# Kernel tuning notes

Measured on AMD Instinct MI355X. Metric: run time of the kernel, lower is better.

The kernel has to match this reference:

```python
import jax, jax.numpy as jnp
import numpy as np

N, E, G, H, F_IN = 100_000, 3_200_000, 256, 16, 7
RRELU_SLOPE = (1.0 / 8.0 + 1.0 / 3.0) / 2.0  # eval-mode RReLU uses mean slope


def rrelu(x):
    return jnp.where(x >= 0, x, RRELU_SLOPE * x)


def gcn_conv(x, edge_index, edge_weight, W, b, n_nodes):
    """PyG GCNConv: add self-loops, symmetric norm, gather-matmul-scatter."""
    row, col = edge_index[0], edge_index[1]
    loop = jnp.arange(n_nodes)
    row = jnp.concatenate([row, loop])
    col = jnp.concatenate([col, loop])
    w = jnp.concatenate([edge_weight, jnp.ones((n_nodes,), x.dtype)])
    deg = jax.ops.segment_sum(w, col, num_segments=n_nodes)
    dis = jnp.where(deg > 0, jax.lax.rsqrt(jnp.maximum(deg, 1e-12)), 0.0)
    norm = dis[row] * w * dis[col]            # [E+N]
    h = x @ W                                  # [N, out]
    msg = h[row] * norm[:, None]               # gather + scale
    return jax.ops.segment_sum(msg, col, num_segments=n_nodes) + b


def max_pool_neighbor_x(x, edge_index, n_nodes):
    row, col = edge_index[0], edge_index[1]
    loop = jnp.arange(n_nodes)
    row = jnp.concatenate([row, loop])
    col = jnp.concatenate([col, loop])
    return jax.ops.segment_max(x[row], col, num_segments=n_nodes)


def setup_inputs() -> dict:
    key = jax.random.key(0)
    ks = jax.random.split(key, 12)
    x = jax.random.normal(ks[0], (N, F_IN), jnp.float32)
    edge_index = jax.random.randint(ks[1], (2, E), 0, N)
    edge_weights = jax.random.uniform(ks[2], (E,), jnp.float32)
    batch = (jnp.arange(N) * G) // N  # sorted, every graph non-empty
    s = 0.2
    W1 = jax.random.normal(ks[3], (F_IN, H), jnp.float32) * s
    b1 = jnp.zeros((H,), jnp.float32)
    W2 = jax.random.normal(ks[4], (H, H), jnp.float32) * s
    b2 = jnp.zeros((H,), jnp.float32)
    Wl1 = jax.random.normal(ks[5], (H, H), jnp.float32) * s
    bl1 = jax.random.normal(ks[6], (H,), jnp.float32) * s
    Wl3 = jax.random.normal(ks[7], (H, H), jnp.float32) * s
    bl3 = jax.random.normal(ks[8], (H,), jnp.float32) * s
    Wl4 = jax.random.normal(ks[9], (H, 1), jnp.float32) * s
    bl4 = jax.random.normal(ks[10], (1,), jnp.float32) * s
    return {"x": x, "edge_index": edge_index, "batch": batch,
            "edge_weights": edge_weights, "W1": W1, "b1": b1, "W2": W2,
            "b2": b2, "Wl1": Wl1, "bl1": bl1, "Wl3": Wl3, "bl3": bl3,
            "Wl4": Wl4, "bl4": bl4}


def reference(x, edge_index, batch, edge_weights, W1, b1, W2, b2,
              Wl1, bl1, Wl3, bl3, Wl4, bl4):
    h = gcn_conv(x, edge_index, edge_weights, W1, b1, N)
    h = max_pool_neighbor_x(h, edge_index, N)
    res = h
    h = gcn_conv(h, edge_index, jnp.ones((E,), h.dtype), W2, b2, N)
    h = jax.nn.relu(res + h)
    g = jax.ops.segment_max(h, batch, num_segments=G)  # global_max_pool
    res = g
    g = rrelu(res + (g @ Wl1 + bl1))
    res = g
    g = rrelu(res + (g @ Wl3 + bl3))
    # dropout p=0.5 in eval mode -> identity
    g = rrelu(g @ Wl4 + bl4)
    return g
```

## Files before the change

### kernel.cpp

```cpp
#include <hip/hip_runtime.h>
#include <hip/hip_fp16.h>
#include <math.h>

#define NN 100000
#define NE 3200000
#define NG 256
#define HD 16
#define FIN 7

#define RB 8
#define RSZ 256
#define NBUK 391
#define NBUKP 400
#define FB 512
#define CHUNK 6250
#define CH2 3125
#define SCB 8
#define ASTRIDE 17
#define CSTRIDE 9
#define LMASK 0x1FFFF

#define S16 65536.0f
#define INV_S16 1.52587890625e-5f
#define IBIAS 33554432u
#define S_DEGW 16777216.0f
#define INV_S_DEGW 5.9604644775390625e-8f

static constexpr float SLOPE = 0.22916666666666666f;

__device__ __forceinline__ float rrelu_f(float a) {
    return a >= 0.f ? a : SLOPE * a;
}

__device__ __forceinline__ unsigned encf(float v) {
    unsigned u = __float_as_uint(v);
    return u ^ (((unsigned)((int)u >> 31)) | 0x80000000u);
}
__device__ __forceinline__ float decf(unsigned u) {
    unsigned m = ((int)u < 0) ? 0x80000000u : 0xFFFFFFFFu;
    return __uint_as_float(u ^ m);
}
#define ENC_NEGINF 0x00800000u

__device__ __forceinline__ float h2f(unsigned short us) {
    __half h = *(__half*)&us;
    return __half2float(h);
}


__global__ __launch_bounds__(512) void k_hist(
        const int* __restrict__ col, int* __restrict__ hist) {
    __shared__ int bins[NBUK];
    for (int i = threadIdx.x; i < NBUK; i += 512) bins[i] = 0;
    __syncthreads();
    const int2* c2 = (const int2*)(col + blockIdx.x * CHUNK);
    for (int i = threadIdx.x; i < CH2; i += 512) {
        int2 v = c2[i];
        atomicAdd(&bins[v.x >> RB], 1);
        atomicAdd(&bins[v.y >> RB], 1);
    }
    __syncthreads();
    for (int i = threadIdx.x; i < NBUK; i += 512)
        hist[blockIdx.x * NBUKP + i] = bins[i];
}

__global__ __launch_bounds__(512) void k_scan_a(
        const int* __restrict__ hist, int* __restrict__ pre_t,
        int* __restrict__ tot) {
    __shared__ int s[SCB * (FB + 1)];
    int t = threadIdx.x;
    int c0 = blockIdx.x * SCB;
    for (int i = t; i < SCB * FB; i += 512) {
        int j = i >> 3, c = i & 7;
        int cc = c0 + c;
        s[c * (FB + 1) + j] = (cc < NBUK) ? hist[j * NBUKP + cc] : 0;
    }
    __syncthreads();
    int w = t >> 6, l = t & 63;
    int* sb = &s[w * (FB + 1)];
    int base = l * 8;
    int loc[8];
    int run = 0;
#pragma unroll
    for (int k = 0; k < 8; ++k) { loc[k] = run; run += sb[base + k]; }
    int inc = run;
#pragma unroll
    for (int d = 1; d < 64; d <<= 1) {
        int v = __shfl_up(inc, d, 64);
        if (l >= d) inc += v;
    }
    int excl = inc - run;
    int cc = c0 + w;
    if (cc < NBUK) {
#pragma unroll
        for (int k = 0; k < 8; ++k) sb[base + k] = excl + loc[k];
        if (l == 63) tot[cc] = inc;
    }
    __syncthreads();
    for (int i = t; i < SCB * FB; i += 512) {
        int j = i >> 3, c = i & 7;
        int cc2 = c0 + c;
        if (cc2 < NBUK) pre_t[j * NBUKP + cc2] = s[c * (FB + 1) + j];
    }
}

__global__ __launch_bounds__(512) void k_scan_b(
        const int* __restrict__ tot, int* __restrict__ bstart,
        unsigned* __restrict__ gbuf) {
    __shared__ int s[512];
    int t = threadIdx.x;
    for (int i = t; i < NG * HD; i += 512) gbuf[i] = 0u;
    int v = (t < NBUK) ? tot[t] : 0;
    s[t] = v;
    __syncthreads();
    for (int d = 1; d < 512; d <<= 1) {
        int add = (t >= d) ? s[t - d] : 0;
        __syncthreads();
        s[t] += add;
        __syncthreads();
    }
    if (t < NBUK) bstart[t + 1] = s[t];
    if (t == 0) bstart[0] = 0;
}

__global__ __launch_bounds__(512) void k_fill(
        const int* __restrict__ row, const int* __restrict__ col,
        const float* __restrict__ ew,
        const int* __restrict__ pre_t, const int* __restrict__ bstart,
        unsigned* __restrict__ sp, unsigned short* __restrict__ swh) {
    __shared__ int lcnt[NBUK];
    __shared__ int gofs[NBUK];
    __shared__ int part[512];
    __shared__ unsigned ssp[CHUNK];
    __shared__ unsigned short ssw[CHUNK];
    __shared__ unsigned short sbuk[CHUNK];
    int t = threadIdx.x;
    for (int i = t; i < NBUK; i += 512) {
        lcnt[i] = 0;
        gofs[i] = bstart[i] + pre_t[blockIdx.x * NBUKP + i];
    }
    __syncthreads();
    const int2* c2 = (const int2*)(col + blockIdx.x * CHUNK);
    const int2* r2 = (const int2*)(row + blockIdx.x * CHUNK);
    const float2* e2 = (const float2*)(ew + blockIdx.x * CHUNK);
    for (int i = t; i < CH2; i += 512) {
        int2 v = c2[i];
        atomicAdd(&lcnt[v.x >> RB], 1);
        atomicAdd(&lcnt[v.y >> RB], 1);
    }
    __syncthreads();
    int c = (t < NBUK) ? lcnt[t] : 0;
    part[t] = c;
    __syncthreads();
    for (int d = 1; d < 512; d <<= 1) {
        int add = (t >= d) ? part[t - d] : 0;
        __syncthreads();
        part[t] += add;
        __syncthreads();
    }
    if (t < NBUK) {
        int e = part[t] - c;
        gofs[t] -= e;
        lcnt[t] = e;
    }
    __syncthreads();
    for (int i = t; i < CH2; i += 512) {
        int2 cv = c2[i];
        int2 rv = r2[i];
        float2 wv = e2[i];
        {
            int b = cv.x >> RB;
            int s = atomicAdd(&lcnt[b], 1);
            ssp[s] = ((unsigned)(cv.x & (RSZ - 1)) << 17) | (unsigned)rv.x;
            __half hv = __float2half_rn(wv.x);
            ssw[s] = *(unsigned short*)&hv;
            sbuk[s] = (unsigned short)b;
        }
        {
            int b = cv.y >> RB;
            int s = atomicAdd(&lcnt[b], 1);
            ssp[s] = ((unsigned)(cv.y & (RSZ - 1)) << 17) | (unsigned)rv.y;
            __half hv = __float2half_rn(wv.y);
            ssw[s] = *(unsigned short*)&hv;
            sbuk[s] = (unsigned short)b;
        }
    }
    __syncthreads();
    for (int s = t; s < CHUNK; s += 512) {
        int g = s + gofs[sbuk[s]];
        sp[g] = ssp[s];
        swh[g] = ssw[s];
    }
}

__global__ __launch_bounds__(1024) void k_deg(
        const unsigned* __restrict__ sp, const unsigned short* __restrict__ swh,
        const int* __restrict__ bstart,
        const float* __restrict__ x, const float* __restrict__ W1,
        float* __restrict__ dis1, float* __restrict__ dis2,
        int* __restrict__ cnts, unsigned* __restrict__ h1h) {
    __shared__ unsigned long long sdeg[RSZ];
    __shared__ float sdis[RSZ];
    __shared__ float sW1[FIN * HD];
    int t = threadIdx.x;
    if (t < FIN * HD) sW1[t] = W1[t];
    if (t < RSZ) sdeg[t] = 0ULL;
    __syncthreads();
    int s0 = bstart[blockIdx.x], s1 = bstart[blockIdx.x + 1];
    int j = s0 + t;
    for (; j + 3072 < s1; j += 4096) {
        unsigned e0 = sp[j], e1 = sp[j + 1024], e2 = sp[j + 2048], e3 = sp[j + 3072];
        float w0 = h2f(swh[j]), w1 = h2f(swh[j + 1024]);
        float w2 = h2f(swh[j + 2048]), w3 = h2f(swh[j + 3072]);
        atomicAdd(&sdeg[e0 >> 17], (1ULL << 32) |
                  (unsigned long long)(unsigned)__float2int_rn(w0 * S_DEGW));
        atomicAdd(&sdeg[e1 >> 17], (1ULL << 32) |
                  (unsigned long long)(unsigned)__float2int_rn(w1 * S_DEGW));
        atomicAdd(&sdeg[e2 >> 17], (1ULL << 32) |
                  (unsigned long long)(unsigned)__float2int_rn(w2 * S_DEGW));
        atomicAdd(&sdeg[e3 >> 17], (1ULL << 32) |
                  (unsigned long long)(unsigned)__float2int_rn(w3 * S_DEGW));
    }
    for (; j < s1; j += 1024) {
        unsigned e = sp[j];
        float w = h2f(swh[j]);
        atomicAdd(&sdeg[e >> 17], (1ULL << 32) |
                  (unsigned long long)(unsigned)__float2int_rn(w * S_DEGW));
    }
    __syncthreads();
    int node0 = blockIdx.x * RSZ;
    if (t < RSZ && node0 + t < NN) {
        unsigned long long v = sdeg[t];
        unsigned cnt = (unsigned)(v >> 32);
        float wsum = (float)(unsigned)(v & 0xFFFFFFFFULL) * INV_S_DEGW;
        float d1 = rsqrtf(wsum + 1.f);
        dis1[node0 + t] = d1;
        sdis[t] = d1;
        dis2[node0 + t] = rsqrtf((float)cnt + 1.f);
        cnts[node0 + t] = (int)cnt;
    }
    __syncthreads();
    for (int i = t; i < RSZ * 8; i += 1024) {
        int ln = i >> 3, p = i & 7;
        int node = node0 + ln;
        if (node < NN) {
            float a0 = 0.f, a1 = 0.f;
#pragma unroll
            for (int k = 0; k < FIN; ++k) {
                float xv = x[node * FIN + k];
                a0 += xv * sW1[k * HD + 2 * p];
                a1 += xv * sW1[k * HD + 2 * p + 1];
            }
            float d = sdis[ln];
            __half2 hh = __floats2half2_rn(a0 * d, a1 * d);
            h1h[node * 8 + p] = *(unsigned*)&hh;
        }
    }
}

__device__ __forceinline__ void conv_acc4(unsigned long long* acc, unsigned ex,
                                          uint4 g, float w, int pb) {
    unsigned long long* a = &acc[(ex >> 17) * CSTRIDE + pb * 4];
    float2 f0 = __half22float2(*(__half2*)&g.x);
    float2 f1 = __half22float2(*(__half2*)&g.y);
    float2 f2 = __half22float2(*(__half2*)&g.z);
    float2 f3 = __half22float2(*(__half2*)&g.w);
    atomicAdd(&a[0], ((unsigned long long)((unsigned)__float2int_rn(f0.x * w) + IBIAS) << 32)
                   |  (unsigned long long)((unsigned)__float2int_rn(f0.y * w) + IBIAS));
    atomicAdd(&a[1], ((unsigned long long)((unsigned)__float2int_rn(f1.x * w) + IBIAS) << 32)
                   |  (unsigned long long)((unsigned)__float2int_rn(f1.y * w) + IBIAS));
    atomicAdd(&a[2], ((unsigned long long)((unsigned)__float2int_rn(f2.x * w) + IBIAS) << 32)
                   |  (unsigned long long)((unsigned)__float2int_rn(f2.y * w) + IBIAS));
    atomicAdd(&a[3], ((unsigned long long)((unsigned)__float2int_rn(f3.x * w) + IBIAS) << 32)
                   |  (unsigned long long)((unsigned)__float2int_rn(f3.y * w) + IBIAS));
}

__global__ __launch_bounds__(1024) void k_conv1(
        const unsigned* __restrict__ sp, const unsigned short* __restrict__ swh,
        const int* __restrict__ bstart,
        const unsigned* __restrict__ h1h, const float* __restrict__ dis1,
        const int* __restrict__ cnts, const float* __restrict__ b1,
        unsigned* __restrict__ h1outh) {
    __shared__ unsigned long long acc[RSZ * CSTRIDE];
    int t = threadIdx.x;
    for (int i = t; i < RSZ * CSTRIDE; i += 1024) acc[i] = 0ULL;
    __syncthreads();
    int pb = t & 1, slot = t >> 1;
    const uint4* h1h4 = (const uint4*)h1h;
    int s0 = bstart[blockIdx.x], s1 = bstart[blockIdx.x + 1];
    int j = s0 + slot;
    for (; j + 1536 < s1; j += 2048) {
        unsigned e0 = sp[j], e1 = sp[j + 512], e2 = sp[j + 1024], e3 = sp[j + 1536];
        float w0 = h2f(swh[j]) * S16, w1 = h2f(swh[j + 512]) * S16;
        float w2 = h2f(swh[j + 1024]) * S16, w3 = h2f(swh[j + 1536]) * S16;
        uint4 g0 = h1h4[(e0 & LMASK) * 2 + pb];
        uint4 g1 = h1h4[(e1 & LMASK) * 2 + pb];
        uint4 g2 = h1h4[(e2 & LMASK) * 2 + pb];
        uint4 g3 = h1h4[(e3 & LMASK) * 2 + pb];
        conv_acc4(acc, e0, g0, w0, pb);
        conv_acc4(acc, e1, g1, w1, pb);
        conv_acc4(acc, e2, g2, w2, pb);
        conv_acc4(acc, e3, g3, w3, pb);
    }
    for (; j < s1; j += 512) {
        unsigned e = sp[j];
        float w = h2f(swh[j]) * S16;
        uint4 g = h1h4[(e & LMASK) * 2 + pb];
        conv_acc4(acc, e, g, w, pb);
    }
    __syncthreads();
    int node0 = blockIdx.x * RSZ;
    for (int i = t; i < RSZ * 8; i += 1024) {
        int ln = i >> 3, pp = i & 7;
        int node = node0 + ln;
        if (node < NN) {
            unsigned long long v = acc[ln * CSTRIDE + pp];
            unsigned kb = (unsigned)cnts[node] * IBIAS;
            float a0 = (float)(int)((unsigned)(v >> 32) - kb) * INV_S16;
            float a1 = (float)(int)((unsigned)(v & 0xFFFFFFFFULL) - kb) * INV_S16;
            float d = dis1[node];
            unsigned sh = h1h[node * 8 + pp];
            float2 sf = __half22float2(*(__half2*)&sh);
            float r0 = (a0 + sf.x) * d + b1[2 * pp];
            float r1 = (a1 + sf.y) * d + b1[2 * pp + 1];
            __half2 hh = __floats2half2_rn(r0, r1);
            h1outh[node * 8 + pp] = *(unsigned*)&hh;
        }
    }
}

__device__ __forceinline__ void pool_acc4(unsigned* acc, unsigned ex,
                                          uint4 g, int pb) {
    unsigned* a = &acc[(ex >> 17) * ASTRIDE + pb * 8];
    float2 f;
    f = __half22float2(*(__half2*)&g.x);
    atomicMax(a + 0, encf(f.x)); atomicMax(a + 1, encf(f.y));
    f = __half22float2(*(__half2*)&g.y);
    atomicMax(a + 2, encf(f.x)); atomicMax(a + 3, encf(f.y));
    f = __half22float2(*(__half2*)&g.z);
    atomicMax(a + 4, encf(f.x)); atomicMax(a + 5, encf(f.y));
    f = __half22float2(*(__half2*)&g.w);
    atomicMax(a + 6, encf(f.x)); atomicMax(a + 7, encf(f.y));
}

__global__ __launch_bounds__(1024) void k_pool_h2(
        const unsigned* __restrict__ sp, const int* __restrict__ bstart,
        const unsigned* __restrict__ h1outh, const float* __restrict__ W2,
        const float* __restrict__ dis2,
        float2* __restrict__ pool2, unsigned* __restrict__ h2sh) {
    __shared__ unsigned acc[RSZ * ASTRIDE];
    __shared__ float sW2[256];
    int t = threadIdx.x;
    if (t < 256) sW2[t] = W2[t];
    for (int i = t; i < RSZ * ASTRIDE; i += 1024) acc[i] = ENC_NEGINF;
    __syncthreads();
    int pb = t & 1, slot = t >> 1;
    const uint4* hv4 = (const uint4*)h1outh;
    int s0 = bstart[blockIdx.x], s1 = bstart[blockIdx.x + 1];
    int j = s0 + slot;
    for (; j + 1536 < s1; j += 2048) {
        unsigned e0 = sp[j], e1 = sp[j + 512], e2 = sp[j + 1024], e3 = sp[j + 1536];
        uint4 g0 = hv4[(e0 & LMASK) * 2 + pb];
        uint4 g1 = hv4[(e1 & LMASK) * 2 + pb];
        uint4 g2 = hv4[(e2 & LMASK) * 2 + pb];
        uint4 g3 = hv4[(e3 & LMASK) * 2 + pb];
        pool_acc4(acc, e0, g0, pb);
        pool_acc4(acc, e1, g1, pb);
        pool_acc4(acc, e2, g2, pb);
        pool_acc4(acc, e3, g3, pb);
    }
    for (; j < s1; j += 512) {
        unsigned e = sp[j];
        uint4 g = hv4[(e & LMASK) * 2 + pb];
        pool_acc4(acc, e, g, pb);
    }
    __syncthreads();
    int node0 = blockIdx.x * RSZ;
    for (int i = t; i < RSZ * 8; i += 1024) {
        int ln = i >> 3, pp = i & 7;
        int node = node0 + ln;
        if (node < NN) {
            unsigned sh = h1outh[node * 8 + pp];
            float2 sf = __half22float2(*(__half2*)&sh);
            float m0 = fmaxf(decf(acc[ln * ASTRIDE + 2 * pp]),     sf.x);
            float m1 = fmaxf(decf(acc[ln * ASTRIDE + 2 * pp + 1]), sf.y);
            pool2[node * 8 + pp] = make_float2(m0, m1);
            acc[ln * ASTRIDE + 2 * pp]     = __float_as_uint(m0);
            acc[ln * ASTRIDE + 2 * pp + 1] = __float_as_uint(m1);
        }
    }
    __syncthreads();
    for (int i = t; i < RSZ * 8; i += 1024) {
        int ln = i >> 3, pp = i & 7;
        int node = node0 + ln;
        if (node < NN) {
            float a0 = 0.f, a1 = 0.f;
#pragma unroll
            for (int k = 0; k < HD; ++k) {
                float pv = __uint_as_float(acc[ln * ASTRIDE + k]);
                a0 += pv * sW2[k * HD + 2 * pp];
                a1 += pv * sW2[k * HD + 2 * pp + 1];
            }
            float d = dis2[node];
            __half2 hh = __floats2half2_rn(a0 * d, a1 * d);
            h2sh[node * 8 + pp] = *(unsigned*)&hh;
        }
    }
}

__global__ __launch_bounds__(1024) void k_conv2(
        const unsigned* __restrict__ sp, const int* __restrict__ bstart,
        const unsigned* __restrict__ h2sh, const float* __restrict__ dis2,
        const int* __restrict__ cnts, const float2* __restrict__ pool2,
        const float* __restrict__ b2, unsigned* __restrict__ gbuf) {
    __shared__ unsigned long long acc[RSZ * CSTRIDE];
    __shared__ unsigned sgmax[4 * HD];
    int t = threadIdx.x;
    for (int i = t; i < RSZ * CSTRIDE; i += 1024) acc[i] = 0ULL;
    if (t < 4 * HD) sgmax[t] = 0u;
    __syncthreads();
    int pb = t & 1, slot = t >> 1;
    const uint4* hv4 = (const uint4*)h2sh;
    int s0 = bstart[blockIdx.x], s1 = bstart[blockIdx.x + 1];
    int j = s0 + slot;
    for (; j + 1536 < s1; j += 2048) {
        unsigned e0 = sp[j], e1 = sp[j + 512], e2 = sp[j + 1024], e3 = sp[j + 1536];
        uint4 g0 = hv4[(e0 & LMASK) * 2 + pb];
        uint4 g1 = hv4[(e1 & LMASK) * 2 + pb];
        uint4 g2 = hv4[(e2 & LMASK) * 2 + pb];
        uint4 g3 = hv4[(e3 & LMASK) * 2 + pb];
        conv_acc4(acc, e0, g0, S16, pb);
        conv_acc4(acc, e1, g1, S16, pb);
        conv_acc4(acc, e2, g2, S16, pb);
        conv_acc4(acc, e3, g3, S16, pb);
    }
    for (; j < s1; j += 512) {
        unsigned e = sp[j];
        uint4 g = hv4[(e & LMASK) * 2 + pb];
        conv_acc4(acc, e, g, S16, pb);
    }
    __syncthreads();
    int node0 = blockIdx.x * RSZ;
    int gbase = (int)(((unsigned long long)node0 * NG) / NN);
    for (int i = t; i < RSZ * 8; i += 1024) {
        int ln = i >> 3, pp = i & 7;
        int node = node0 + ln;
        if (node < NN) {
            unsigned long long v = acc[ln * CSTRIDE + pp];
            unsigned kb = (unsigned)cnts[node] * IBIAS;
            float a0 = (float)(int)((unsigned)(v >> 32) - kb) * INV_S16;
            float a1 = (float)(int)((unsigned)(v & 0xFFFFFFFFULL) - kb) * INV_S16;
            float d = dis2[node];
            unsigned sh = h2sh[node * 8 + pp];
            float2 self = __half22float2(*(__half2*)&sh);
            float2 pl = pool2[node * 8 + pp];
            float r0 = fmaxf(pl.x + (a0 + self.x) * d + b2[2 * pp], 0.f);
            float r1 = fmaxf(pl.y + (a1 + self.y) * d + b2[2 * pp + 1], 0.f);
            int lg = (int)(((unsigned long long)node * NG) / NN) - gbase;
            atomicMax(&sgmax[lg * HD + 2 * pp],     __float_as_uint(r0));
            atomicMax(&sgmax[lg * HD + 2 * pp + 1], __float_as_uint(r1));
        }
    }
    __syncthreads();
    if (t < 4 * HD) {
        int lg = t >> 4, f = t & 15;
        int g = gbase + lg;
        unsigned m = sgmax[t];
        if (g < NG && m > 0u) atomicMax(&gbuf[g * HD + f], m);
    }
}

__global__ __launch_bounds__(256) void k_mlp(
        const float* __restrict__ gbuf,
        const float* __restrict__ Wl1, const float* __restrict__ bl1,
        const float* __restrict__ Wl3, const float* __restrict__ bl3,
        const float* __restrict__ Wl4, const float* __restrict__ bl4,
        float* __restrict__ out) {
    __shared__ float sW1[256], sW3[256], sW4[16], sb1[16], sb3[16];
    __shared__ float sb4;
    int tid = threadIdx.x;
    sW1[tid] = Wl1[tid];
    sW3[tid] = Wl3[tid];
    if (tid < 16) { sW4[tid] = Wl4[tid]; sb1[tid] = bl1[tid]; sb3[tid] = bl3[tid]; }
    if (tid == 0) sb4 = bl4[0];
    __syncthreads();

    float v[16], t1[16], t2[16];
#pragma unroll
    for (int f = 0; f < 16; ++f) v[f] = gbuf[tid * 16 + f];
#pragma unroll
    for (int f = 0; f < 16; ++f) {
        float a = sb1[f] + v[f];
#pragma unroll
        for (int k = 0; k < 16; ++k) a += v[k] * sW1[k * 16 + f];
        t1[f] = rrelu_f(a);
    }
#pragma unroll
    for (int f = 0; f < 16; ++f) {
        float a = sb3[f] + t1[f];
#pragma unroll
        for (int k = 0; k < 16; ++k) a += t1[k] * sW3[k * 16 + f];
        t2[f] = rrelu_f(a);
    }
    float o = sb4;
#pragma unroll
    for (int k = 0; k < 16; ++k) o += t2[k] * sW4[k];
    out[tid] = rrelu_f(o);
}

extern "C" void kernel_launch(void* const* d_in, const int* in_sizes, int n_in,
                              void* d_out, int out_size, void* d_ws, size_t ws_size,
                              hipStream_t stream) {
    const float* x   = (const float*)d_in[0];
    const int*   ei  = (const int*)  d_in[1];
    const float* ew  = (const float*)d_in[3];
    const float* W1  = (const float*)d_in[4];
    const float* b1  = (const float*)d_in[5];
    const float* W2  = (const float*)d_in[6];
    const float* b2  = (const float*)d_in[7];
    const float* Wl1 = (const float*)d_in[8];
    const float* bl1 = (const float*)d_in[9];
    const float* Wl3 = (const float*)d_in[10];
    const float* bl3 = (const float*)d_in[11];
    const float* Wl4 = (const float*)d_in[12];
    const float* bl4 = (const float*)d_in[13];
    const int* row = ei;
    const int* col = ei + NE;

    float* ws = (float*)d_ws;
    float* pool  = ws;
    float* dead  = pool + NN * HD;
    float* dis1  = dead + NN * HD;
    float* dis2  = dis1 + NN;
    int*   cnts  = (int*)(dis2 + NN);
    unsigned* gbuf = (unsigned*)(cnts + NN);
    unsigned* h1h    = gbuf   + NG * HD;
    unsigned* h1outh = h1h    + NN * 8;
    unsigned* h2sh   = h1outh + NN * 8;
    unsigned* sp     = h2sh   + NN * 8;
    unsigned short* swh = (unsigned short*)(sp + NE);
    int* tot    = (int*)(swh + NE + (NE & 1));
    int* bstart = tot + NBUK;
    int* hist   = (int*)pool;
    int* pre_t  = (int*)dead;

    k_hist     <<<FB, 512, 0, stream>>>(col, hist);
    k_scan_a   <<<(NBUK + SCB - 1) / SCB, 512, 0, stream>>>(hist, pre_t, tot);
    k_scan_b   <<<1, 512, 0, stream>>>(tot, bstart, gbuf);
    k_fill     <<<FB, 512, 0, stream>>>(row, col, ew, pre_t, bstart, sp, swh);
    k_deg      <<<NBUK, 1024, 0, stream>>>(sp, swh, bstart, x, W1,
                                           dis1, dis2, cnts, h1h);
    k_conv1    <<<NBUK, 1024, 0, stream>>>(sp, swh, bstart, h1h, dis1,
                                           cnts, b1, h1outh);
    k_pool_h2  <<<NBUK, 1024, 0, stream>>>(sp, bstart, h1outh, W2, dis2,
                                           (float2*)pool, h2sh);
    k_conv2    <<<NBUK, 1024, 0, stream>>>(sp, bstart, h2sh, dis2, cnts,
                                           (const float2*)pool, b2, gbuf);
    k_mlp      <<<1, 256, 0, stream>>>((const float*)gbuf, Wl1, bl1, Wl3, bl3,
                                       Wl4, bl4, (float*)d_out);
}
```

Before: 219.8 us.

## Build per-node CSR in degree kernel and use gather-based segment reductions

```diff
diff --git a/kernel.cpp b/kernel.cpp
--- a/kernel.cpp
+++ b/kernel.cpp
@@ -16,13 +16,12 @@
 #define CHUNK 6250
 #define CH2 3125
 #define SCB 8
-#define ASTRIDE 17
-#define CSTRIDE 9
 #define LMASK 0x1FFFF
 
-#define S16 65536.0f
-#define INV_S16 1.52587890625e-5f
-#define IBIAS 33554432u
+#define SEGN 64
+#define SEGB 1563
+#define PSTRIDE 17
+
 #define S_DEGW 16777216.0f
 #define INV_S_DEGW 5.9604644775390625e-8f
 
@@ -31,16 +30,6 @@
 __device__ __forceinline__ float rrelu_f(float a) {
     return a >= 0.f ? a : SLOPE * a;
 }
-
-__device__ __forceinline__ unsigned encf(float v) {
-    unsigned u = __float_as_uint(v);
-    return u ^ (((unsigned)((int)u >> 31)) | 0x80000000u);
-}
-__device__ __forceinline__ float decf(unsigned u) {
-    unsigned m = ((int)u < 0) ? 0x80000000u : 0xFFFFFFFFu;
-    return __uint_as_float(u ^ m);
-}
-#define ENC_NEGINF 0x00800000u
 
 __device__ __forceinline__ float h2f(unsigned short us) {
     __half h = *(__half*)&us;
@@ -198,10 +187,13 @@
         const int* __restrict__ bstart,
         const float* __restrict__ x, const float* __restrict__ W1,
         float* __restrict__ dis1, float* __restrict__ dis2,
-        int* __restrict__ cnts, unsigned* __restrict__ h1h) {
+        int* __restrict__ nstart, unsigned* __restrict__ h1h,
+        unsigned* __restrict__ sp2, unsigned short* __restrict__ swh2) {
     __shared__ unsigned long long sdeg[RSZ];
     __shared__ float sdis[RSZ];
     __shared__ float sW1[FIN * HD];
+    __shared__ int sscan[RSZ];
+    __shared__ int lrank[RSZ];
     int t = threadIdx.x;
     if (t < FIN * HD) sW1[t] = W1[t];
     if (t < RSZ) sdeg[t] = 0ULL;
@@ -229,17 +221,36 @@
     }
     __syncthreads();
     int node0 = blockIdx.x * RSZ;
-    if (t < RSZ && node0 + t < NN) {
-        unsigned long long v = sdeg[t];
-        unsigned cnt = (unsigned)(v >> 32);
-        float wsum = (float)(unsigned)(v & 0xFFFFFFFFULL) * INV_S_DEGW;
-        float d1 = rsqrtf(wsum + 1.f);
-        dis1[node0 + t] = d1;
-        sdis[t] = d1;
-        dis2[node0 + t] = rsqrtf((float)cnt + 1.f);
-        cnts[node0 + t] = (int)cnt;
-    }
-    __syncthreads();
+    int cnt_t = 0;
+    if (t < RSZ) { cnt_t = (int)(sdeg[t] >> 32); sscan[t] = cnt_t; }
+    __syncthreads();
+    for (int d = 1; d < RSZ; d <<= 1) {
+        int add = (t < RSZ && t >= d) ? sscan[t - d] : 0;
+        __syncthreads();
+        if (t < RSZ) sscan[t] += add;
+        __syncthreads();
+    }
+    if (t < RSZ) {
+        int excl = sscan[t] - cnt_t;
+        lrank[t] = s0 + excl;
+        if (node0 + t <= NN) nstart[node0 + t] = s0 + excl;
+        if (node0 + t < NN) {
+            unsigned long long v = sdeg[t];
+            unsigned cnt = (unsigned)(v >> 32);
+            float wsum = (float)(unsigned)(v & 0xFFFFFFFFULL) * INV_S_DEGW;
+            float d1 = rsqrtf(wsum + 1.f);
+            dis1[node0 + t] = d1;
+            sdis[t] = d1;
+            dis2[node0 + t] = rsqrtf((float)cnt + 1.f);
+        }
+    }
+    __syncthreads();
+    for (int k = s0 + t; k < s1; k += 1024) {
+        unsigned e = sp[k];
+        int pos = atomicAdd(&lrank[e >> 17], 1);
+        sp2[pos] = e & LMASK;
+        swh2[pos] = swh[k];
+    }
     for (int i = t; i < RSZ * 8; i += 1024) {
         int ln = i >> 3, p = i & 7;
         int node = node0 + ln;
@@ -258,146 +269,104 @@
     }
 }
 
-__device__ __forceinline__ void conv_acc4(unsigned long long* acc, unsigned ex,
-                                          uint4 g, float w, int pb) {
-    unsigned long long* a = &acc[(ex >> 17) * CSTRIDE + pb * 4];
-    float2 f0 = __half22float2(*(__half2*)&g.x);
-    float2 f1 = __half22float2(*(__half2*)&g.y);
-    float2 f2 = __half22float2(*(__half2*)&g.z);
-    float2 f3 = __half22float2(*(__half2*)&g.w);
-    atomicAdd(&a[0], ((unsigned long long)((unsigned)__float2int_rn(f0.x * w) + IBIAS) << 32)
-                   |  (unsigned long long)((unsigned)__float2int_rn(f0.y * w) + IBIAS));
-    atomicAdd(&a[1], ((unsigned long long)((unsigned)__float2int_rn(f1.x * w) + IBIAS) << 32)
-                   |  (unsigned long long)((unsigned)__float2int_rn(f1.y * w) + IBIAS));
-    atomicAdd(&a[2], ((unsigned long long)((unsigned)__float2int_rn(f2.x * w) + IBIAS) << 32)
-                   |  (unsigned long long)((unsigned)__float2int_rn(f2.y * w) + IBIAS));
-    atomicAdd(&a[3], ((unsigned long long)((unsigned)__float2int_rn(f3.x * w) + IBIAS) << 32)
-                   |  (unsigned long long)((unsigned)__float2int_rn(f3.y * w) + IBIAS));
-}
-
-__global__ __launch_bounds__(1024) void k_conv1(
-        const unsigned* __restrict__ sp, const unsigned short* __restrict__ swh,
-        const int* __restrict__ bstart,
+__global__ __launch_bounds__(256) void k_conv1(
+        const unsigned* __restrict__ sp2, const unsigned short* __restrict__ swh2,
+        const int* __restrict__ nstart,
         const unsigned* __restrict__ h1h, const float* __restrict__ dis1,
-        const int* __restrict__ cnts, const float* __restrict__ b1,
-        unsigned* __restrict__ h1outh) {
-    __shared__ unsigned long long acc[RSZ * CSTRIDE];
-    int t = threadIdx.x;
-    for (int i = t; i < RSZ * CSTRIDE; i += 1024) acc[i] = 0ULL;
-    __syncthreads();
-    int pb = t & 1, slot = t >> 1;
-    const uint4* h1h4 = (const uint4*)h1h;
-    int s0 = bstart[blockIdx.x], s1 = bstart[blockIdx.x + 1];
-    int j = s0 + slot;
-    for (; j + 1536 < s1; j += 2048) {
-        unsigned e0 = sp[j], e1 = sp[j + 512], e2 = sp[j + 1024], e3 = sp[j + 1536];
-        float w0 = h2f(swh[j]) * S16, w1 = h2f(swh[j + 512]) * S16;
-        float w2 = h2f(swh[j + 1024]) * S16, w3 = h2f(swh[j + 1536]) * S16;
-        uint4 g0 = h1h4[(e0 & LMASK) * 2 + pb];
-        uint4 g1 = h1h4[(e1 & LMASK) * 2 + pb];
-        uint4 g2 = h1h4[(e2 & LMASK) * 2 + pb];
-        uint4 g3 = h1h4[(e3 & LMASK) * 2 + pb];
-        conv_acc4(acc, e0, g0, w0, pb);
-        conv_acc4(acc, e1, g1, w1, pb);
-        conv_acc4(acc, e2, g2, w2, pb);
-        conv_acc4(acc, e3, g3, w3, pb);
-    }
-    for (; j < s1; j += 512) {
-        unsigned e = sp[j];
-        float w = h2f(swh[j]) * S16;
-        uint4 g = h1h4[(e & LMASK) * 2 + pb];
-        conv_acc4(acc, e, g, w, pb);
-    }
-    __syncthreads();
-    int node0 = blockIdx.x * RSZ;
-    for (int i = t; i < RSZ * 8; i += 1024) {
-        int ln = i >> 3, pp = i & 7;
-        int node = node0 + ln;
+        const float* __restrict__ b1, unsigned* __restrict__ h1outh) {
+    int t = threadIdx.x;
+    int p = t & 7, g = t >> 3;
+    float bb0 = b1[2 * p], bb1 = b1[2 * p + 1];
+    int nbase = blockIdx.x * SEGN;
+#pragma unroll
+    for (int rep = 0; rep < 2; ++rep) {
+        int node = nbase + g + rep * 32;
         if (node < NN) {
-            unsigned long long v = acc[ln * CSTRIDE + pp];
-            unsigned kb = (unsigned)cnts[node] * IBIAS;
-            float a0 = (float)(int)((unsigned)(v >> 32) - kb) * INV_S16;
-            float a1 = (float)(int)((unsigned)(v & 0xFFFFFFFFULL) - kb) * INV_S16;
+            int e0 = nstart[node], e1 = nstart[node + 1];
+            float a0 = 0.f, a1 = 0.f;
+            int j = e0;
+            for (; j + 3 < e1; j += 4) {
+                unsigned r0 = sp2[j],     r1 = sp2[j + 1];
+                unsigned r2 = sp2[j + 2], r3 = sp2[j + 3];
+                float w0 = h2f(swh2[j]),     w1 = h2f(swh2[j + 1]);
+                float w2 = h2f(swh2[j + 2]), w3 = h2f(swh2[j + 3]);
+                unsigned g0 = h1h[r0 * 8 + p], g1 = h1h[r1 * 8 + p];
+                unsigned g2 = h1h[r2 * 8 + p], g3 = h1h[r3 * 8 + p];
+                float2 f;
+                f = __half22float2(*(__half2*)&g0); a0 += f.x * w0; a1 += f.y * w0;
+                f = __half22float2(*(__half2*)&g1); a0 += f.x * w1; a1 += f.y * w1;
+                f = __half22float2(*(__half2*)&g2); a0 += f.x * w2; a1 += f.y * w2;
+                f = __half22float2(*(__half2*)&g3); a0 += f.x * w3; a1 += f.y * w3;
+            }
+            for (; j < e1; ++j) {
+                unsigned r = sp2[j];
+                float w = h2f(swh2[j]);
+                unsigned gv = h1h[r * 8 + p];
+                float2 f = __half22float2(*(__half2*)&gv);
+                a0 += f.x * w; a1 += f.y * w;
+            }
             float d = dis1[node];
-            unsigned sh = h1h[node * 8 + pp];
+            unsigned sh = h1h[node * 8 + p];
             float2 sf = __half22float2(*(__half2*)&sh);
-            float r0 = (a0 + sf.x) * d + b1[2 * pp];
-            float r1 = (a1 + sf.y) * d + b1[2 * pp + 1];
-            __half2 hh = __floats2half2_rn(r0, r1);
-            h1outh[node * 8 + pp] = *(unsigned*)&hh;
-        }
-    }
-}
-
-__device__ __forceinline__ void pool_acc4(unsigned* acc, unsigned ex,
-                                          uint4 g, int pb) {
-    unsigned* a = &acc[(ex >> 17) * ASTRIDE + pb * 8];
-    float2 f;
-    f = __half22float2(*(__half2*)&g.x);
-    atomicMax(a + 0, encf(f.x)); atomicMax(a + 1, encf(f.y));
-    f = __half22float2(*(__half2*)&g.y);
-    atomicMax(a + 2, encf(f.x)); atomicMax(a + 3, encf(f.y));
-    f = __half22float2(*(__half2*)&g.z);
-    atomicMax(a + 4, encf(f.x)); atomicMax(a + 5, encf(f.y));
-    f = __half22float2(*(__half2*)&g.w);
-    atomicMax(a + 6, encf(f.x)); atomicMax(a + 7, encf(f.y));
-}
-
-__global__ __launch_bounds__(1024) void k_pool_h2(
-        const unsigned* __restrict__ sp, const int* __restrict__ bstart,
+            float r0o = (a0 + sf.x) * d + bb0;
+            float r1o = (a1 + sf.y) * d + bb1;
+            __half2 hh = __floats2half2_rn(r0o, r1o);
+            h1outh[node * 8 + p] = *(unsigned*)&hh;
+        }
+    }
+}
+
+__global__ __launch_bounds__(256) void k_pool_h2(
+        const unsigned* __restrict__ sp2, const int* __restrict__ nstart,
         const unsigned* __restrict__ h1outh, const float* __restrict__ W2,
         const float* __restrict__ dis2,
         float2* __restrict__ pool2, unsigned* __restrict__ h2sh) {
-    __shared__ unsigned acc[RSZ * ASTRIDE];
+    __shared__ float spool[SEGN * PSTRIDE];
     __shared__ float sW2[256];
     int t = threadIdx.x;
-    if (t < 256) sW2[t] = W2[t];
-    for (int i = t; i < RSZ * ASTRIDE; i += 1024) acc[i] = ENC_NEGINF;
-    __syncthreads();
-    int pb = t & 1, slot = t >> 1;
-    const uint4* hv4 = (const uint4*)h1outh;
-    int s0 = bstart[blockIdx.x], s1 = bstart[blockIdx.x + 1];
-    int j = s0 + slot;
-    for (; j + 1536 < s1; j += 2048) {
-        unsigned e0 = sp[j], e1 = sp[j + 512], e2 = sp[j + 1024], e3 = sp[j + 1536];
-        uint4 g0 = hv4[(e0 & LMASK) * 2 + pb];
-        uint4 g1 = hv4[(e1 & LMASK) * 2 + pb];
-        uint4 g2 = hv4[(e2 & LMASK) * 2 + pb];
-        uint4 g3 = hv4[(e3 & LMASK) * 2 + pb];
-        pool_acc4(acc, e0, g0, pb);
-        pool_acc4(acc, e1, g1, pb);
-        pool_acc4(acc, e2, g2, pb);
-        pool_acc4(acc, e3, g3, pb);
-    }
-    for (; j < s1; j += 512) {
-        unsigned e = sp[j];
-        uint4 g = hv4[(e & LMASK) * 2 + pb];
-        pool_acc4(acc, e, g, pb);
-    }
-    __syncthreads();
-    int node0 = blockIdx.x * RSZ;
-    for (int i = t; i < RSZ * 8; i += 1024) {
+    sW2[t] = W2[t];
+    int p = t & 7, g = t >> 3;
+    int nbase = blockIdx.x * SEGN;
+#pragma unroll
+    for (int rep = 0; rep < 2; ++rep) {
+        int ln = g + rep * 32;
+        int node = nbase + ln;
+        if (node < NN) {
+            unsigned sh = h1outh[node * 8 + p];
+            float2 sf = __half22float2(*(__half2*)&sh);
+            float m0 = sf.x, m1 = sf.y;
+            int e0 = nstart[node], e1 = nstart[node + 1];
+            int j = e0;
+            for (; j + 3 < e1; j += 4) {
+                unsigned r0 = sp2[j],     r1 = sp2[j + 1];
+                unsigned r2 = sp2[j + 2], r3 = sp2[j + 3];
+                unsigned g0 = h1outh[r0 * 8 + p], g1 = h1outh[r1 * 8 + p];
+                unsigned g2 = h1outh[r2 * 8 + p], g3 = h1outh[r3 * 8 + p];
+                float2 f;
+                f = __half22float2(*(__half2*)&g0); m0 = fmaxf(m0, f.x); m1 = fmaxf(m1, f.y);
+                f = __half22float2(*(__half2*)&g1); m0 = fmaxf(m0, f.x); m1 = fmaxf(m1, f.y);
+                f = __half22float2(*(__half2*)&g2); m0 = fmaxf(m0, f.x); m1 = fmaxf(m1, f.y);
+                f = __half22float2(*(__half2*)&g3); m0 = fmaxf(m0, f.x); m1 = fmaxf(m1, f.y);
+            }
+            for (; j < e1; ++j) {
+                unsigned gv = h1outh[sp2[j] * 8 + p];
+                float2 f = __half22float2(*(__half2*)&gv);
+                m0 = fmaxf(m0, f.x); m1 = fmaxf(m1, f.y);
+            }
+            pool2[node * 8 + p] = make_float2(m0, m1);
+            spool[ln * PSTRIDE + 2 * p]     = m0;
+            spool[ln * PSTRIDE + 2 * p + 1] = m1;
+        }
+    }
+    __syncthreads();
+    for (int i = t; i < SEGN * 8; i += 256) {
         int ln = i >> 3, pp = i & 7;
-        int node = node0 + ln;
-        if (node < NN) {
-            unsigned sh = h1outh[node * 8 + pp];
-            float2 sf = __half22float2(*(__half2*)&sh);
-            float m0 = fmaxf(decf(acc[ln * ASTRIDE + 2 * pp]),     sf.x);
-            float m1 = fmaxf(decf(acc[ln * ASTRIDE + 2 * pp + 1]), sf.y);
-            pool2[node * 8 + pp] = make_float2(m0, m1);
-            acc[ln * ASTRIDE + 2 * pp]     = __float_as_uint(m0);
-            acc[ln * ASTRIDE + 2 * pp + 1] = __float_as_uint(m1);
-        }
-    }
-    __syncthreads();
-    for (int i = t; i < RSZ * 8; i += 1024) {
-        int ln = i >> 3, pp = i & 7;
-        int node = node0 + ln;
+        int node = nbase + ln;
         if (node < NN) {
             float a0 = 0.f, a1 = 0.f;
 #pragma unroll
             for (int k = 0; k < HD; ++k) {
-                float pv = __uint_as_float(acc[ln * ASTRIDE + k]);
+                float pv = spool[ln * PSTRIDE + k];
                 a0 += pv * sW2[k * HD + 2 * pp];
                 a1 += pv * sW2[k * HD + 2 * pp + 1];
             }
@@ -408,65 +377,59 @@
     }
 }
 
-__global__ __launch_bounds__(1024) void k_conv2(
-        const unsigned* __restrict__ sp, const int* __restrict__ bstart,
+__global__ __launch_bounds__(256) void k_conv2(
+        const unsigned* __restrict__ sp2, const int* __restrict__ nstart,
         const unsigned* __restrict__ h2sh, const float* __restrict__ dis2,
-        const int* __restrict__ cnts, const float2* __restrict__ pool2,
-        const float* __restrict__ b2, unsigned* __restrict__ gbuf) {
-    __shared__ unsigned long long acc[RSZ * CSTRIDE];
+        const float2* __restrict__ pool2, const float* __restrict__ b2,
+        unsigned* __restrict__ gbuf) {
     __shared__ unsigned sgmax[4 * HD];
     int t = threadIdx.x;
-    for (int i = t; i < RSZ * CSTRIDE; i += 1024) acc[i] = 0ULL;
     if (t < 4 * HD) sgmax[t] = 0u;
     __syncthreads();
-    int pb = t & 1, slot = t >> 1;
-    const uint4* hv4 = (const uint4*)h2sh;
-    int s0 = bstart[blockIdx.x], s1 = bstart[blockIdx.x + 1];
-    int j = s0 + slot;
-    for (; j + 1536 < s1; j += 2048) {
-        unsigned e0 = sp[j], e1 = sp[j + 512], e2 = sp[j + 1024], e3 = sp[j + 1536];
-        uint4 g0 = hv4[(e0 & LMASK) * 2 + pb];
-        uint4 g1 = hv4[(e1 & LMASK) * 2 + pb];
-        uint4 g2 = hv4[(e2 & LMASK) * 2 + pb];
-        uint4 g3 = hv4[(e3 & LMASK) * 2 + pb];
-        conv_acc4(acc, e0, g0, S16, pb);
-        conv_acc4(acc, e1, g1, S16, pb);
-        conv_acc4(acc, e2, g2, S16, pb);
-        conv_acc4(acc, e3, g3, S16, pb);
-    }
-    for (; j < s1; j += 512) {
-        unsigned e = sp[j];
-        uint4 g = hv4[(e & LMASK) * 2 + pb];
-        conv_acc4(acc, e, g, S16, pb);
-    }
-    __syncthreads();
-    int node0 = blockIdx.x * RSZ;
-    int gbase = (int)(((unsigned long long)node0 * NG) / NN);
-    for (int i = t; i < RSZ * 8; i += 1024) {
-        int ln = i >> 3, pp = i & 7;
-        int node = node0 + ln;
+    int p = t & 7, g = t >> 3;
+    float bb0 = b2[2 * p], bb1 = b2[2 * p + 1];
+    int nbase = blockIdx.x * SEGN;
+    int gbase = (int)(((unsigned long long)nbase * NG) / NN);
+#pragma unroll
+    for (int rep = 0; rep < 2; ++rep) {
+        int node = nbase + g + rep * 32;
         if (node < NN) {
-            unsigned long long v = acc[ln * CSTRIDE + pp];
-            unsigned kb = (unsigned)cnts[node] * IBIAS;
-            float a0 = (float)(int)((unsigned)(v >> 32) - kb) * INV_S16;
-            float a1 = (float)(int)((unsigned)(v & 0xFFFFFFFFULL) - kb) * INV_S16;
+            int e0 = nstart[node], e1 = nstart[node + 1];
+            float a0 = 0.f, a1 = 0.f;
+            int j = e0;
+            for (; j + 3 < e1; j += 4) {
+                unsigned r0 = sp2[j],     r1 = sp2[j + 1];
+                unsigned r2 = sp2[j + 2], r3 = sp2[j + 3];
+                unsigned g0 = h2sh[r0 * 8 + p], g1 = h2sh[r1 * 8 + p];
+                unsigned g2 = h2sh[r2 * 8 + p], g3 = h2sh[r3 * 8 + p];
+                float2 f;
+                f = __half22float2(*(__half2*)&g0); a0 += f.x; a1 += f.y;
+                f = __half22float2(*(__half2*)&g1); a0 += f.x; a1 += f.y;
+                f = __half22float2(*(__half2*)&g2); a0 += f.x; a1 += f.y;
+                f = __half22float2(*(__half2*)&g3); a0 += f.x; a1 += f.y;
+            }
+            for (; j < e1; ++j) {
+                unsigned gv = h2sh[sp2[j] * 8 + p];
+                float2 f = __half22float2(*(__half2*)&gv);
+                a0 += f.x; a1 += f.y;
+            }
             float d = dis2[node];
-            unsigned sh = h2sh[node * 8 + pp];
+            unsigned sh = h2sh[node * 8 + p];
             float2 self = __half22float2(*(__half2*)&sh);
-            float2 pl = pool2[node * 8 + pp];
-            float r0 = fmaxf(pl.x + (a0 + self.x) * d + b2[2 * pp], 0.f);
-            float r1 = fmaxf(pl.y + (a1 + self.y) * d + b2[2 * pp + 1], 0.f);
+            float2 pl = pool2[node * 8 + p];
+            float r0o = fmaxf(pl.x + (a0 + self.x) * d + bb0, 0.f);
+            float r1o = fmaxf(pl.y + (a1 + self.y) * d + bb1, 0.f);
             int lg = (int)(((unsigned long long)node * NG) / NN) - gbase;
-            atomicMax(&sgmax[lg * HD + 2 * pp],     __float_as_uint(r0));
-            atomicMax(&sgmax[lg * HD + 2 * pp + 1], __float_as_uint(r1));
+            atomicMax(&sgmax[lg * HD + 2 * p],     __float_as_uint(r0o));
+            atomicMax(&sgmax[lg * HD + 2 * p + 1], __float_as_uint(r1o));
         }
     }
     __syncthreads();
     if (t < 4 * HD) {
         int lg = t >> 4, f = t & 15;
-        int g = gbase + lg;
+        int gg = gbase + lg;
         unsigned m = sgmax[t];
-        if (g < NG && m > 0u) atomicMax(&gbuf[g * HD + f], m);
+        if (gg < NG && m > 0u) atomicMax(&gbuf[gg * HD + f], m);
     }
 }
 
@@ -532,14 +495,16 @@
     float* dead  = pool + NN * HD;
     float* dis1  = dead + NN * HD;
     float* dis2  = dis1 + NN;
-    int*   cnts  = (int*)(dis2 + NN);
-    unsigned* gbuf = (unsigned*)(cnts + NN);
+    int*   nstart = (int*)(dis2 + NN);
+    unsigned* gbuf = (unsigned*)(nstart + NN + 2);
     unsigned* h1h    = gbuf   + NG * HD;
     unsigned* h1outh = h1h    + NN * 8;
     unsigned* h2sh   = h1outh + NN * 8;
     unsigned* sp     = h2sh   + NN * 8;
     unsigned short* swh = (unsigned short*)(sp + NE);
-    int* tot    = (int*)(swh + NE + (NE & 1));
+    unsigned* sp2    = (unsigned*)(swh + NE);
+    unsigned short* swh2 = (unsigned short*)(sp2 + NE);
+    int* tot    = (int*)(swh2 + NE);
     int* bstart = tot + NBUK;
     int* hist   = (int*)pool;
     int* pre_t  = (int*)dead;
@@ -549,13 +514,13 @@
     k_scan_b   <<<1, 512, 0, stream>>>(tot, bstart, gbuf);
     k_fill     <<<FB, 512, 0, stream>>>(row, col, ew, pre_t, bstart, sp, swh);
     k_deg      <<<NBUK, 1024, 0, stream>>>(sp, swh, bstart, x, W1,
-                                           dis1, dis2, cnts, h1h);
-    k_conv1    <<<NBUK, 1024, 0, stream>>>(sp, swh, bstart, h1h, dis1,
-                                           cnts, b1, h1outh);
-    k_pool_h2  <<<NBUK, 1024, 0, stream>>>(sp, bstart, h1outh, W2, dis2,
-                                           (float2*)pool, h2sh);
-    k_conv2    <<<NBUK, 1024, 0, stream>>>(sp, bstart, h2sh, dis2, cnts,
-                                           (const float2*)pool, b2, gbuf);
+                                           dis1, dis2, nstart, h1h, sp2, swh2);
+    k_conv1    <<<SEGB, 256, 0, stream>>>(sp2, swh2, nstart, h1h, dis1,
+                                          b1, h1outh);
+    k_pool_h2  <<<SEGB, 256, 0, stream>>>(sp2, nstart, h1outh, W2, dis2,
+                                          (float2*)pool, h2sh);
+    k_conv2    <<<SEGB, 256, 0, stream>>>(sp2, nstart, h2sh, dis2,
+                                          (const float2*)pool, b2, gbuf);
     k_mlp      <<<1, 256, 0, stream>>>((const float*)gbuf, Wl1, bl1, Wl3, bl3,
                                        Wl4, bl4, (float*)d_out);
 }
```

New measurement: 279.2 us. 27.0% more time.
